# Optimization experiments

Hardware: AMD Instinct MI355X
Metric: run time of the kernel (lower is better)

## Reference

```python
import jax, jax.numpy as jnp
import numpy as np

# Static config mirroring FinalFFTAudioEngine(compression_ratio=0.3)
COMPRESSION_RATIO = 0.3
ENERGY_THRESHOLD = 0.05
WINDOW = 256  # window_size=512 -> power-of-2 loop ends at 512 -> min(512//2, 512) = 256


def _important_mask(energy, min_count, threshold):
    """Threshold mask, replaced by top-k mask if too few survive (faithful to torch code)."""
    th_mask = energy > threshold
    _, idx = jax.lax.top_k(energy, min_count)
    tk_mask = jnp.zeros(energy.shape, dtype=bool).at[idx].set(True)
    return jnp.where(jnp.sum(th_mask) < min_count, tk_mask, th_mask)


def setup_inputs() -> dict:
    key = jax.random.key(0)
    weight_matrix = jax.random.normal(key, (4096, 4096), dtype=jnp.float32)
    return {"weight_matrix": weight_matrix}


def reference(weight_matrix):
    # weight_to_audio_signal: flatten + max-abs normalize
    signal = weight_matrix.reshape(-1).astype(jnp.float32)
    n = signal.shape[0]  # 16777216, exact multiple of WINDOW -> no padding branch
    sig_max = jnp.max(jnp.abs(signal))
    norm = jnp.where(sig_max > 1e-10, sig_max, jnp.float32(1.0))
    signal = signal / norm

    # optimized_spectral_analysis: non-overlapping windows + per-window FFT
    windows = signal.reshape(-1, WINDOW)          # [T, F] = [65536, 256]
    spec = jnp.fft.fft(windows)                   # complex64 [T, F]

    # intelligent_frequency_selection
    energy = jnp.abs(spec) ** 2                   # [T, F]
    freq_energy = jnp.mean(energy, axis=0)        # [F]
    time_energy = jnp.mean(energy, axis=1)        # [T]
    min_freqs = max(1, int(WINDOW * (1.0 - COMPRESSION_RATIO * 0.7)))          # 202
    min_times = max(1, int(windows.shape[0] * (1.0 - COMPRESSION_RATIO * 0.7)))  # 51773
    freq_mask = _important_mask(freq_energy, min_freqs,
                                ENERGY_THRESHOLD * jnp.max(freq_energy))
    time_mask = _important_mask(time_energy, min_times,
                                ENERGY_THRESHOLD * jnp.max(time_energy))

    # lossless_compression: fused masked copy (replaces nested python double-for-loop)
    mask2d = time_mask[:, None] & freq_mask[None, :]
    compressed = jnp.where(mask2d, spec, jnp.zeros((), dtype=spec.dtype))

    # perfect_reconstruction: IFFT, take real part, flatten, trim to original length
    recon = jnp.real(jnp.fft.ifft(compressed)).reshape(-1)[:n]
    return recon
```

## Files before the change

kernel.cpp:

```cpp
#include <hip/hip_runtime.h>

#define N_TOTAL   16777216
#define NWIN      65536
#define MIN_FREQS 202
#define MIN_TIMES 51773
#define NBLK      256

#define IDX_TCNT    2
#define IDX_FMALL   3
#define IDX_INVNORM 5
#define IDX_FCNT    6
#define IDX_FMASK   8
#define IDX_SLOTS   264
#define IDX_AMAXB   65800
#define IDX_TMAXB   66056
#define IDX_SUMSQ   66312
#define IDX_TMASKA  131848

typedef __attribute__((ext_vector_type(8)))  short bf16x8;
typedef __attribute__((ext_vector_type(16))) float f32x16;

__device__ __forceinline__ float dpp_row_sum16(float x)
{
    x += __int_as_float(__builtin_amdgcn_mov_dpp(__float_as_int(x), 0xB1,  0xF, 0xF, true));
    x += __int_as_float(__builtin_amdgcn_mov_dpp(__float_as_int(x), 0x4E,  0xF, 0xF, true));
    x += __int_as_float(__builtin_amdgcn_mov_dpp(__float_as_int(x), 0x141, 0xF, 0xF, true));
    x += __int_as_float(__builtin_amdgcn_mov_dpp(__float_as_int(x), 0x140, 0xF, 0xF, true));
    return x;
}

__device__ __forceinline__ unsigned short bf16r(float v)
{
    unsigned u = __float_as_uint(v);
    return (unsigned short)((u + 0x7FFFu + ((u >> 16) & 1u)) >> 16);
}
__device__ __forceinline__ unsigned bfpair(float a, float b)
{
    return (unsigned)bf16r(a) | ((unsigned)bf16r(b) << 16);
}

__device__ __forceinline__ void do_stage(short (*Ab)[264], const float4 v0, const float4 v1,
                                         int wrow, int scol, float* sumsq_g,
                                         float& amax, float& tmx)
{
    amax = fmaxf(amax, fmaxf(fmaxf(fabsf(v0.x), fabsf(v0.y)),
                             fmaxf(fabsf(v0.z), fabsf(v0.w))));
    amax = fmaxf(amax, fmaxf(fmaxf(fabsf(v1.x), fabsf(v1.y)),
                             fmaxf(fabsf(v1.z), fabsf(v1.w))));
    float ss = v0.x*v0.x + v0.y*v0.y + v0.z*v0.z + v0.w*v0.w
             + v1.x*v1.x + v1.y*v1.y + v1.z*v1.z + v1.w*v1.w;
    ss = dpp_row_sum16(ss);
    ss += __shfl_xor(ss, 16);
    if (scol == 0) { sumsq_g[wrow] = ss; tmx = fmaxf(tmx, ss); }
    uint4 u;
    u.x = bfpair(v0.x, v0.y); u.y = bfpair(v0.z, v0.w);
    u.z = bfpair(v1.x, v1.y); u.w = bfpair(v1.z, v1.w);
    *(uint4*)&Ab[wrow][scol * 8] = u;
}

__global__ __launch_bounds__(1024) void k_stats(const float* __restrict__ x,
                                                float* __restrict__ W)
{
    __shared__ short Abuf[2][32][264];
    __shared__ float red[1024];
    __shared__ float sE[512];
    const int tid  = threadIdx.x;
    const int lane = tid & 63;
    const int wv   = tid >> 6;
    const int hi   = lane >> 5;
    const int col  = lane & 31;
    const int wrow = tid >> 5;
    const int scol = tid & 31;

    bf16x8 F[16];
    {
        const int f = ((wv & 7) << 5) + col;
        const bool use_sin = (wv >= 8);
#pragma unroll
        for (int kc = 0; kc < 16; ++kc) {
            bf16x8 t;
#pragma unroll
            for (int j = 0; j < 8; ++j) {
                const int n = kc * 16 + hi * 8 + j;
                const int m = (n * f) & 255;
                float s, c;
                __sincosf((float)m * 0.024543692606170f, &s, &c);
                t[j] = (short)bf16r(use_sin ? s : c);
            }
            F[kc] = t;
        }
    }

    const int b = blockIdx.x;
    const float* xb = x + ((size_t)b << 16);
    float* sumsq = W + IDX_SUMSQ + (b << 8);
    float amax = 0.f, tmx = 0.f, fsum = 0.f;

    float4 v0, v1;
    {
        const float4* p = (const float4*)(xb + tid * 8);
        v0 = p[0]; v1 = p[1];
    }
    do_stage(Abuf[0], v0, v1, wrow, scol, sumsq, amax, tmx);
    __syncthreads();

    int cur = 0;
#pragma unroll 1
    for (int g = 0; g < 8; ++g) {
        if (g < 7) {
            const float4* p = (const float4*)(xb + (g + 1) * 8192 + tid * 8);
            v0 = p[0]; v1 = p[1];
        }
        f32x16 acc;
#pragma unroll
        for (int r = 0; r < 16; ++r) acc[r] = 0.f;
#pragma unroll
        for (int kc = 0; kc < 16; ++kc) {
            const bf16x8 af = *(const bf16x8*)&Abuf[cur][col][kc * 16 + hi * 8];
            acc = __builtin_amdgcn_mfma_f32_32x32x16_bf16(af, F[kc], acc, 0, 0, 0);
        }
#pragma unroll
        for (int r = 0; r < 16; ++r) fsum += acc[r] * acc[r];
        if (g < 7)
            do_stage(Abuf[cur ^ 1], v0, v1, wrow, scol, sumsq + (g + 1) * 32, amax, tmx);
        __syncthreads();
        cur ^= 1;
    }

    fsum += __shfl_xor(fsum, 32);
    if (lane < 32)
        sE[((wv >= 8) ? 256 : 0) + ((wv & 7) << 5) + col] = fsum;
    __syncthreads();
    if (tid < 256)
        W[IDX_SLOTS + (size_t)b * 256 + tid] = sE[tid] + sE[256 + tid];
    if (b == 0 && tid == 0) ((int*)W)[IDX_TCNT] = 0;

    red[tid] = amax; __syncthreads();
    for (int s = 512; s > 0; s >>= 1) {
        if (tid < s) red[tid] = fmaxf(red[tid], red[tid + s]);
        __syncthreads();
    }
    if (tid == 0) W[IDX_AMAXB + b] = red[0];
    __syncthreads();
    red[tid] = tmx; __syncthreads();
    for (int s = 512; s > 0; s >>= 1) {
        if (tid < s) red[tid] = fmaxf(red[tid], red[tid + s]);
        __syncthreads();
    }
    if (tid == 0) W[IDX_TMAXB + b] = red[0];
}

__global__ __launch_bounds__(256) void k_post(float* __restrict__ W)
{
    __shared__ float red[256];
    const int tid = threadIdx.x;

    if (blockIdx.x != 0) {
        float tm = W[IDX_TMAXB + tid];
        red[tid] = tm; __syncthreads();
        for (int s = 128; s > 0; s >>= 1) {
            if (tid < s) red[tid] = fmaxf(red[tid], red[tid + s]);
            __syncthreads();
        }
        const float tthr = 0.05f * red[0];
        __syncthreads();
        const float* sumsq = W + IDX_SUMSQ;
        float* tmask = W + IDX_TMASKA;
        const int base = (blockIdx.x - 1) * 1024 + tid;
        int c = 0;
#pragma unroll
        for (int k = 0; k < 4; k++) {
            const int i = base + k * 256;
            const int mm = (sumsq[i] > tthr) ? 1 : 0;
            c += mm;
            tmask[i] = (float)mm;
        }
        red[tid] = (float)c; __syncthreads();
        for (int s = 128; s > 0; s >>= 1) {
            if (tid < s) red[tid] += red[tid + s];
            __syncthreads();
        }
        if (tid == 0) atomicAdd((int*)W + IDX_TCNT, (int)red[0]);
        return;
    }

    __shared__ float e[256];
    float am = W[IDX_AMAXB + tid];
    red[tid] = am; __syncthreads();
    for (int s = 128; s > 0; s >>= 1) {
        if (tid < s) red[tid] = fmaxf(red[tid], red[tid + s]);
        __syncthreads();
    }
    const float amax = red[0];
    __syncthreads();

    float acc = 0.f;
#pragma unroll 8
    for (int s = 0; s < NBLK; s++) acc += W[IDX_SLOTS + (size_t)s * 256 + tid];
    e[tid] = acc;
    red[tid] = acc; __syncthreads();
    for (int s = 128; s > 0; s >>= 1) {
        if (tid < s) red[tid] = fmaxf(red[tid], red[tid + s]);
        __syncthreads();
    }
    const float fthr = 0.05f * red[0];
    __syncthreads();
    const int my = (acc > fthr) ? 1 : 0;
    red[tid] = (float)my; __syncthreads();
    for (int s = 128; s > 0; s >>= 1) {
        if (tid < s) red[tid] += red[tid + s];
        __syncthreads();
    }
    const int fcnt = (int)red[0];
    __syncthreads();
    float m;
    if (fcnt >= MIN_FREQS) {
        m = (float)my;
    } else {
        int rank = 0;
        for (int j = 0; j < 256; j++) {
            const float ej = e[j];
            if (ej > acc || (ej == acc && j < tid)) rank++;
        }
        m = (rank < MIN_FREQS) ? 1.f : 0.f;
    }
    W[IDX_FMASK + tid] = m;
    red[tid] = m; __syncthreads();
    for (int s = 128; s > 0; s >>= 1) {
        if (tid < s) red[tid] += red[tid + s];
        __syncthreads();
    }
    if (tid == 0) {
        ((int*)W)[IDX_FMALL] = ((int)red[0] == 256) ? 1 : 0;
        ((int*)W)[IDX_FCNT]  = fcnt;
        W[IDX_INVNORM] = 1.f / ((amax > 1e-10f) ? amax : 1.f);
    }
}

__global__ __launch_bounds__(256) void k_timefb(float* __restrict__ W)
{
    if (((const int*)W)[IDX_TCNT] >= MIN_TIMES) return;
    const int t = blockIdx.x * 256 + threadIdx.x;
    const float* sumsq = W + IDX_SUMSQ;
    const float st = sumsq[t];
    int rank = 0;
    for (int j = 0; j < NWIN; j++) {
        const float sj = sumsq[j];
        if (sj > st || (sj == st && j < t)) rank++;
    }
    W[IDX_TMASKA + t] = (rank < MIN_TIMES) ? 1.f : 0.f;
}

__global__ __launch_bounds__(256) void k_out(const float* __restrict__ x,
                                             float* __restrict__ out,
                                             const float* __restrict__ W)
{
    const int tid = threadIdx.x;
    const int fm_all = ((const int*)W)[IDX_FMALL];
    const float inv_norm = W[IDX_INVNORM];
    if (fm_all) {
        const float4* xi = (const float4*)x;
        float4* yo = (float4*)out;
        const float* tmask = W + IDX_TMASKA;
        for (int i = blockIdx.x * 256 + tid; i < N_TOTAL / 4; i += gridDim.x * 256) {
            const float s = inv_norm * tmask[i >> 6];
            float4 v = xi[i];
            v.x *= s; v.y *= s; v.z *= s; v.w *= s;
            yo[i] = v;
        }
        return;
    }
    __shared__ float re[256], im[256], twr[128], twi[128], fm[256];
    if (tid < 128) {
        float s, c;
        __sincosf(-6.283185307179586f * (float)tid / 256.0f, &s, &c);
        twr[tid] = c; twi[tid] = s;
    }
    fm[tid] = W[IDX_FMASK + (int)(__brev((unsigned)tid) >> 24)];
    __syncthreads();
    const float scale = inv_norm * (1.f / 256.f);
    for (int w = blockIdx.x; w < NWIN; w += gridDim.x) {
        const float tm = W[IDX_TMASKA + w];
        if (tm == 0.f) { out[w * 256 + tid] = 0.f; continue; }
        re[tid] = x[w * 256 + tid]; im[tid] = 0.f;
        __syncthreads();
        for (int lh = 7; lh >= 0; lh--) {
            const int half = 1 << lh;
            if (tid < 128) {
                const int k  = tid & (half - 1);
                const int i0 = ((tid & ~(half - 1)) << 1) | k;
                const int i1 = i0 + half;
                const float ar = re[i0], ai = im[i0], br = re[i1], bi = im[i1];
                const float dr = ar - br, di = ai - bi;
                re[i0] = ar + br; im[i0] = ai + bi;
                const int ti = k << (7 - lh);
                const float wr = twr[ti], wi = twi[ti];
                re[i1] = dr * wr - di * wi;
                im[i1] = dr * wi + di * wr;
            }
            __syncthreads();
        }
        re[tid] *= fm[tid]; im[tid] *= fm[tid];
        __syncthreads();
        for (int lh = 0; lh < 8; lh++) {
            const int half = 1 << lh;
            if (tid < 128) {
                const int k  = tid & (half - 1);
                const int i0 = ((tid & ~(half - 1)) << 1) | k;
                const int i1 = i0 + half;
                const int ti = k << (7 - lh);
                const float wr = twr[ti], wi = -twi[ti];
                const float br = re[i1], bi = im[i1];
                const float tr = br * wr - bi * wi;
                const float ts = br * wi + bi * wr;
                const float ar = re[i0], ai = im[i0];
                re[i1] = ar - tr; im[i1] = ai - ts;
                re[i0] = ar + tr; im[i0] = ai + ts;
            }
            __syncthreads();
        }
        out[w * 256 + tid] = re[tid] * scale;
        __syncthreads();
    }
}

extern "C" void kernel_launch(void* const* d_in, const int* in_sizes, int n_in,
                              void* d_out, int out_size, void* d_ws, size_t ws_size,
                              hipStream_t stream)
{
    const float* x = (const float*)d_in[0];
    float* out = (float*)d_out;
    float* W = (float*)d_ws;
    hipLaunchKernelGGL(k_stats,  dim3(NBLK), dim3(1024), 0, stream, x, W);
    hipLaunchKernelGGL(k_post,   dim3(65),   dim3(256),  0, stream, W);
    hipLaunchKernelGGL(k_timefb, dim3(256),  dim3(256),  0, stream, W);
    hipLaunchKernelGGL(k_out,    dim3(2048), dim3(256),  0, stream, x, out, W);
}
```

Before: 74.19 us.

## Fuse stats, mask, fallback and output kernels into one cooperative kernel

Merges the four separate launches (stats, post-processing, time fallback, output) into a single kernel launched cooperatively. Phases are separated by grid-wide syncs. The post-processing work is spread across all blocks, and block 0 handles the frequency mask. This removes the launch gaps and the tail/ramp costs between kernels. In exchange, the output pass is limited to 256 blocks of 1024 threads, and each grid sync adds its own barrier cost.

```diff
diff --git a/kernel.cpp b/kernel.cpp
--- a/kernel.cpp
+++ b/kernel.cpp
@@ -1,4 +1,7 @@
 #include <hip/hip_runtime.h>
+#include <hip/hip_cooperative_groups.h>
+
+namespace cg = cooperative_groups;
 
 #define N_TOTAL   16777216
 #define NWIN      65536
@@ -58,12 +61,15 @@
     *(uint4*)&Ab[wrow][scol * 8] = u;
 }
 
-__global__ __launch_bounds__(1024) void k_stats(const float* __restrict__ x,
-                                                float* __restrict__ W)
+__global__ __launch_bounds__(1024) void k_all(const float* __restrict__ x,
+                                              float* __restrict__ out,
+                                              float* __restrict__ W)
 {
     __shared__ short Abuf[2][32][264];
     __shared__ float red[1024];
     __shared__ float sE[512];
+    __shared__ float reS[256], imS[256], twrS[128], twiS[128], fmS[256];
+
     const int tid  = threadIdx.x;
     const int lane = tid & 63;
     const int wv   = tid >> 6;
@@ -71,6 +77,7 @@
     const int col  = lane & 31;
     const int wrow = tid >> 5;
     const int scol = tid & 31;
+    const int b    = blockIdx.x;
 
     bf16x8 F[16];
     {
@@ -91,7 +98,6 @@
         }
     }
 
-    const int b = blockIdx.x;
     const float* xb = x + ((size_t)b << 16);
     float* sumsq = W + IDX_SUMSQ + (b << 8);
     float amax = 0.f, tmx = 0.f, fsum = 0.f;
@@ -148,121 +154,113 @@
         __syncthreads();
     }
     if (tid == 0) W[IDX_TMAXB + b] = red[0];
-}
-
-__global__ __launch_bounds__(256) void k_post(float* __restrict__ W)
-{
-    __shared__ float red[256];
-    const int tid = threadIdx.x;
-
-    if (blockIdx.x != 0) {
-        float tm = W[IDX_TMAXB + tid];
-        red[tid] = tm; __syncthreads();
+
+    cg::this_grid().sync();
+
+    red[tid] = (tid < 256) ? W[IDX_TMAXB + tid] : 0.f;
+    __syncthreads();
+    for (int s = 128; s > 0; s >>= 1) {
+        if (tid < s) red[tid] = fmaxf(red[tid], red[tid + s]);
+        __syncthreads();
+    }
+    const float tthr = 0.05f * red[0];
+    __syncthreads();
+    int mm = 0;
+    if (tid < 256) {
+        const int i = (b << 8) + tid;
+        mm = (W[IDX_SUMSQ + i] > tthr) ? 1 : 0;
+        W[IDX_TMASKA + i] = (float)mm;
+    }
+    red[tid] = (float)mm; __syncthreads();
+    for (int s = 512; s > 0; s >>= 1) {
+        if (tid < s) red[tid] += red[tid + s];
+        __syncthreads();
+    }
+    if (tid == 0) atomicAdd((int*)W + IDX_TCNT, (int)red[0]);
+
+    if (b == 0) {
+        red[tid] = (tid < 256) ? W[IDX_AMAXB + tid] : 0.f;
+        __syncthreads();
         for (int s = 128; s > 0; s >>= 1) {
             if (tid < s) red[tid] = fmaxf(red[tid], red[tid + s]);
             __syncthreads();
         }
-        const float tthr = 0.05f * red[0];
-        __syncthreads();
-        const float* sumsq = W + IDX_SUMSQ;
-        float* tmask = W + IDX_TMASKA;
-        const int base = (blockIdx.x - 1) * 1024 + tid;
-        int c = 0;
-#pragma unroll
-        for (int k = 0; k < 4; k++) {
-            const int i = base + k * 256;
-            const int mm = (sumsq[i] > tthr) ? 1 : 0;
-            c += mm;
-            tmask[i] = (float)mm;
-        }
-        red[tid] = (float)c; __syncthreads();
+        const float amax_g = red[0];
+        __syncthreads();
+        float acc = 0.f;
+        for (int s = (tid >> 8); s < NBLK; s += 4)
+            acc += W[IDX_SLOTS + (size_t)s * 256 + (tid & 255)];
+        if (tid < 512) sE[tid] = 0.f;
+        __syncthreads();
+        atomicAdd(&sE[tid & 255], acc);
+        __syncthreads();
+        red[tid] = (tid < 256) ? sE[tid] : 0.f;
+        __syncthreads();
         for (int s = 128; s > 0; s >>= 1) {
+            if (tid < s) red[tid] = fmaxf(red[tid], red[tid + s]);
+            __syncthreads();
+        }
+        const float fthr = 0.05f * red[0];
+        __syncthreads();
+        const int my = (tid < 256 && sE[tid] > fthr) ? 1 : 0;
+        red[tid] = (float)my; __syncthreads();
+        for (int s = 512; s > 0; s >>= 1) {
             if (tid < s) red[tid] += red[tid + s];
             __syncthreads();
         }
-        if (tid == 0) atomicAdd((int*)W + IDX_TCNT, (int)red[0]);
-        return;
-    }
-
-    __shared__ float e[256];
-    float am = W[IDX_AMAXB + tid];
-    red[tid] = am; __syncthreads();
-    for (int s = 128; s > 0; s >>= 1) {
-        if (tid < s) red[tid] = fmaxf(red[tid], red[tid + s]);
-        __syncthreads();
-    }
-    const float amax = red[0];
-    __syncthreads();
-
-    float acc = 0.f;
-#pragma unroll 8
-    for (int s = 0; s < NBLK; s++) acc += W[IDX_SLOTS + (size_t)s * 256 + tid];
-    e[tid] = acc;
-    red[tid] = acc; __syncthreads();
-    for (int s = 128; s > 0; s >>= 1) {
-        if (tid < s) red[tid] = fmaxf(red[tid], red[tid + s]);
-        __syncthreads();
-    }
-    const float fthr = 0.05f * red[0];
-    __syncthreads();
-    const int my = (acc > fthr) ? 1 : 0;
-    red[tid] = (float)my; __syncthreads();
-    for (int s = 128; s > 0; s >>= 1) {
-        if (tid < s) red[tid] += red[tid + s];
-        __syncthreads();
-    }
-    const int fcnt = (int)red[0];
-    __syncthreads();
-    float m;
-    if (fcnt >= MIN_FREQS) {
-        m = (float)my;
-    } else {
-        int rank = 0;
-        for (int j = 0; j < 256; j++) {
-            const float ej = e[j];
-            if (ej > acc || (ej == acc && j < tid)) rank++;
-        }
-        m = (rank < MIN_FREQS) ? 1.f : 0.f;
-    }
-    W[IDX_FMASK + tid] = m;
-    red[tid] = m; __syncthreads();
-    for (int s = 128; s > 0; s >>= 1) {
-        if (tid < s) red[tid] += red[tid + s];
-        __syncthreads();
-    }
-    if (tid == 0) {
-        ((int*)W)[IDX_FMALL] = ((int)red[0] == 256) ? 1 : 0;
-        ((int*)W)[IDX_FCNT]  = fcnt;
-        W[IDX_INVNORM] = 1.f / ((amax > 1e-10f) ? amax : 1.f);
-    }
-}
-
-__global__ __launch_bounds__(256) void k_timefb(float* __restrict__ W)
-{
-    if (((const int*)W)[IDX_TCNT] >= MIN_TIMES) return;
-    const int t = blockIdx.x * 256 + threadIdx.x;
-    const float* sumsq = W + IDX_SUMSQ;
-    const float st = sumsq[t];
-    int rank = 0;
-    for (int j = 0; j < NWIN; j++) {
-        const float sj = sumsq[j];
-        if (sj > st || (sj == st && j < t)) rank++;
-    }
-    W[IDX_TMASKA + t] = (rank < MIN_TIMES) ? 1.f : 0.f;
-}
-
-__global__ __launch_bounds__(256) void k_out(const float* __restrict__ x,
-                                             float* __restrict__ out,
-                                             const float* __restrict__ W)
-{
-    const int tid = threadIdx.x;
+        const int fcnt = (int)red[0];
+        __syncthreads();
+        float m = 0.f;
+        if (tid < 256) {
+            if (fcnt >= MIN_FREQS) {
+                m = (float)my;
+            } else {
+                int rank = 0;
+                for (int j = 0; j < 256; j++) {
+                    const float ej = sE[j];
+                    if (ej > sE[tid] || (ej == sE[tid] && j < tid)) rank++;
+                }
+                m = (rank < MIN_FREQS) ? 1.f : 0.f;
+            }
+            W[IDX_FMASK + tid] = m;
+        }
+        red[tid] = m; __syncthreads();
+        for (int s = 512; s > 0; s >>= 1) {
+            if (tid < s) red[tid] += red[tid + s];
+            __syncthreads();
+        }
+        if (tid == 0) {
+            ((int*)W)[IDX_FMALL] = ((int)red[0] == 256) ? 1 : 0;
+            ((int*)W)[IDX_FCNT]  = fcnt;
+            W[IDX_INVNORM] = 1.f / ((amax_g > 1e-10f) ? amax_g : 1.f);
+        }
+    }
+
+    cg::this_grid().sync();
+
+    const int tcnt = ((const int*)W)[IDX_TCNT];
+    if (tcnt < MIN_TIMES) {
+        if (tid < 256) {
+            const int t = (b << 8) + tid;
+            const float st = W[IDX_SUMSQ + t];
+            int rank = 0;
+            for (int j = 0; j < NWIN; j++) {
+                const float sj = W[IDX_SUMSQ + j];
+                if (sj > st || (sj == st && j < t)) rank++;
+            }
+            W[IDX_TMASKA + t] = (rank < MIN_TIMES) ? 1.f : 0.f;
+        }
+        cg::this_grid().sync();
+    }
+
     const int fm_all = ((const int*)W)[IDX_FMALL];
     const float inv_norm = W[IDX_INVNORM];
     if (fm_all) {
         const float4* xi = (const float4*)x;
         float4* yo = (float4*)out;
         const float* tmask = W + IDX_TMASKA;
-        for (int i = blockIdx.x * 256 + tid; i < N_TOTAL / 4; i += gridDim.x * 256) {
+#pragma unroll 4
+        for (int i = b * 1024 + tid; i < N_TOTAL / 4; i += NBLK * 1024) {
             const float s = inv_norm * tmask[i >> 6];
             float4 v = xi[i];
             v.x *= s; v.y *= s; v.z *= s; v.w *= s;
@@ -270,19 +268,22 @@
         }
         return;
     }
-    __shared__ float re[256], im[256], twr[128], twi[128], fm[256];
     if (tid < 128) {
         float s, c;
         __sincosf(-6.283185307179586f * (float)tid / 256.0f, &s, &c);
-        twr[tid] = c; twi[tid] = s;
-    }
-    fm[tid] = W[IDX_FMASK + (int)(__brev((unsigned)tid) >> 24)];
+        twrS[tid] = c; twiS[tid] = s;
+    }
+    if (tid < 256)
+        fmS[tid] = W[IDX_FMASK + (int)(__brev((unsigned)tid) >> 24)];
     __syncthreads();
     const float scale = inv_norm * (1.f / 256.f);
-    for (int w = blockIdx.x; w < NWIN; w += gridDim.x) {
+    for (int w = b; w < NWIN; w += NBLK) {
         const float tm = W[IDX_TMASKA + w];
-        if (tm == 0.f) { out[w * 256 + tid] = 0.f; continue; }
-        re[tid] = x[w * 256 + tid]; im[tid] = 0.f;
+        if (tm == 0.f) {
+            if (tid < 256) out[w * 256 + tid] = 0.f;
+            continue;
+        }
+        if (tid < 256) { reS[tid] = x[w * 256 + tid]; imS[tid] = 0.f; }
         __syncthreads();
         for (int lh = 7; lh >= 0; lh--) {
             const int half = 1 << lh;
@@ -290,17 +291,17 @@
                 const int k  = tid & (half - 1);
                 const int i0 = ((tid & ~(half - 1)) << 1) | k;
                 const int i1 = i0 + half;
-                const float ar = re[i0], ai = im[i0], br = re[i1], bi = im[i1];
+                const float ar = reS[i0], ai = imS[i0], br = reS[i1], bi = imS[i1];
                 const float dr = ar - br, di = ai - bi;
-                re[i0] = ar + br; im[i0] = ai + bi;
+                reS[i0] = ar + br; imS[i0] = ai + bi;
                 const int ti = k << (7 - lh);
-                const float wr = twr[ti], wi = twi[ti];
-                re[i1] = dr * wr - di * wi;
-                im[i1] = dr * wi + di * wr;
-            }
-            __syncthreads();
-        }
-        re[tid] *= fm[tid]; im[tid] *= fm[tid];
+                const float wr = twrS[ti], wi = twiS[ti];
+                reS[i1] = dr * wr - di * wi;
+                imS[i1] = dr * wi + di * wr;
+            }
+            __syncthreads();
+        }
+        if (tid < 256) { reS[tid] *= fmS[tid]; imS[tid] *= fmS[tid]; }
         __syncthreads();
         for (int lh = 0; lh < 8; lh++) {
             const int half = 1 << lh;
@@ -309,17 +310,17 @@
                 const int i0 = ((tid & ~(half - 1)) << 1) | k;
                 const int i1 = i0 + half;
                 const int ti = k << (7 - lh);
-                const float wr = twr[ti], wi = -twi[ti];
-                const float br = re[i1], bi = im[i1];
+                const float wr = twrS[ti], wi = -twiS[ti];
+                const float br = reS[i1], bi = imS[i1];
                 const float tr = br * wr - bi * wi;
                 const float ts = br * wi + bi * wr;
-                const float ar = re[i0], ai = im[i0];
-                re[i1] = ar - tr; im[i1] = ai - ts;
-                re[i0] = ar + tr; im[i0] = ai + ts;
-            }
-            __syncthreads();
-        }
-        out[w * 256 + tid] = re[tid] * scale;
+                const float ar = reS[i0], ai = imS[i0];
+                reS[i1] = ar - tr; imS[i1] = ai - ts;
+                reS[i0] = ar + tr; imS[i0] = ai + ts;
+            }
+            __syncthreads();
+        }
+        if (tid < 256) out[w * 256 + tid] = reS[tid] * scale;
         __syncthreads();
     }
 }
@@ -331,8 +332,7 @@
     const float* x = (const float*)d_in[0];
     float* out = (float*)d_out;
     float* W = (float*)d_ws;
-    hipLaunchKernelGGL(k_stats,  dim3(NBLK), dim3(1024), 0, stream, x, W);
-    hipLaunchKernelGGL(k_post,   dim3(65),   dim3(256),  0, stream, W);
-    hipLaunchKernelGGL(k_timefb, dim3(256),  dim3(256),  0, stream, W);
-    hipLaunchKernelGGL(k_out,    dim3(2048), dim3(256),  0, stream, x, out, W);
-}
+    void* args[] = { (void*)&x, (void*)&out, (void*)&W };
+    hipLaunchCooperativeKernel((const void*)k_all, dim3(NBLK), dim3(1024),
+                               args, 0, stream);
+}
```

New measurement: 131.7 us. +77.5%, slower.
